# Kernel tuning notes

Hardware: AMD Instinct MI355X
Metric: run time of the kernel (lower is better)

Reference implementation:

```python
import jax, jax.numpy as jnp
import numpy as np

FEAT_DIM = 2048
H_DIM = 1024
N = 8192  # num_obj (tree nodes in pre-order traversal order)


def setup_inputs() -> dict:
    key = jax.random.key(0)
    ks = jax.random.split(key, 5)
    features = jax.random.normal(ks[0], (N, FEAT_DIM), dtype=jnp.float32)
    # block_orthogonal init approximated by scaled gaussian (same math at runtime)
    Wx = jax.random.normal(ks[1], (4 * H_DIM, FEAT_DIM), dtype=jnp.float32) / np.sqrt(FEAT_DIM)
    Wh = jax.random.normal(ks[2], (4 * H_DIM, H_DIM), dtype=jnp.float32) / np.sqrt(H_DIM)
    bx = jnp.zeros((4 * H_DIM,), dtype=jnp.float32)
    # iofuh bias: forget-gate block [2h:3h] filled with 1.0
    bh = jnp.zeros((4 * H_DIM,), dtype=jnp.float32).at[2 * H_DIM:3 * H_DIM].set(1.0)
    # binary tree in pre-order-compatible (topological) order: parent of t is (t-1)//2 < t; root = -1
    t = jnp.arange(N)
    parent_idx = jnp.where(t == 0, -1, (t - 1) // 2).astype(jnp.int32)
    root_c = jax.random.normal(ks[3], (1, H_DIM), dtype=jnp.float32)
    root_h = jax.random.normal(ks[4], (1, H_DIM), dtype=jnp.float32)
    return {"features": features, "Wx": Wx, "bx": bx, "Wh": Wh, "bh": bh,
            "parent_idx": parent_idx, "root_c": root_c, "root_h": root_h}


def reference(features, Wx, bx, Wh, bh, parent_idx, root_c, root_h):
    # Precompute the input projection for ALL nodes with one big GEMM
    # (the original does this per-node; math is identical).
    xproj = features @ Wx.T + (bx + bh)  # [N, 4H]
    WhT = Wh.T  # [H, 4H]
    # state buffers; slot 0 holds the root state, slot t+1 holds node t's state
    h_buf = jnp.concatenate([root_h, jnp.zeros((N, H_DIM), features.dtype)], axis=0)  # [N+1, H]
    c_buf = jnp.concatenate([root_c, jnp.zeros((N, H_DIM), features.dtype)], axis=0)

    def step(carry, inp):
        h_buf, c_buf = carry
        t, p, xp = inp
        hp = h_buf[p + 1]  # parent hidden [H]
        cp = c_buf[p + 1]  # parent cell   [H]
        iofu = xp + hp @ WhT  # [4H]
        i, o, f, u = jnp.split(iofu, 4)
        i = jax.nn.sigmoid(i)
        o = jax.nn.sigmoid(o)
        f = jax.nn.sigmoid(f)
        u = jnp.tanh(u)
        c = i * u + f * cp
        h = o * jnp.tanh(c)
        h_buf = h_buf.at[t + 1].set(h)
        c_buf = c_buf.at[t + 1].set(c)
        return (h_buf, c_buf), h

    ts = jnp.arange(N)
    (_, _), hidden = jax.lax.scan(step, (h_buf, c_buf), (ts, parent_idx, xproj))
    return hidden  # [N, H] == treelstm_io.hidden rows in traversal order
```

## Files before the change

kernel.cpp:

```cpp
#include <hip/hip_runtime.h>
#include <math.h>

#define FEAT 2048
#define HD 1024
#define FH 4096
#define NN 8192

using s16x8 = __attribute__((ext_vector_type(8))) short;
using f32x4 = __attribute__((ext_vector_type(4))) float;

#define GLOBAL_AS __attribute__((address_space(1)))
#define LDS_AS __attribute__((address_space(3)))

__device__ __forceinline__ void gload_lds16(const void* g, void* l) {
    __builtin_amdgcn_global_load_lds((const GLOBAL_AS unsigned int*)g,
                                     (LDS_AS unsigned int*)l, 16, 0, 0);
}

__device__ __forceinline__ unsigned short f2bf(float f) {
    union { float f; unsigned u; } v; v.f = f;
    unsigned r = v.u + 0x7FFFu + ((v.u >> 16) & 1u);
    return (unsigned short)(r >> 16);
}

__device__ __forceinline__ float fast_sig(float x) { return 1.0f / (1.0f + __expf(-x)); }
__device__ __forceinline__ float fast_tanh(float x) {
    float ax = fabsf(x);
    float e = __expf(2.0f * ax);
    float r = 1.0f - 2.0f / (e + 1.0f);
    return copysignf(r, x);
}

__global__ __launch_bounds__(256) void convert_all_kernel(
    const float* __restrict__ feat, const float* __restrict__ Wx,
    const float* __restrict__ Wh, unsigned short* __restrict__ feat_b,
    unsigned short* __restrict__ Wx_b, unsigned short* __restrict__ Wh_b)
{
    const size_t n1 = (size_t)NN * FEAT;
    const size_t n2 = n1 + (size_t)FH * FEAT;
    size_t i = ((size_t)blockIdx.x * 256 + threadIdx.x) * 8;
    const float* s; unsigned short* d;
    if (i < n1)      { s = feat + i;        d = feat_b + i; }
    else if (i < n2) { s = Wx + (i - n1);   d = Wx_b + (i - n1); }
    else             { s = Wh + (i - n2);   d = Wh_b + (i - n2); }
    float4 a = *(const float4*)s;
    float4 b = *(const float4*)(s + 4);
    unsigned short r[8] = {f2bf(a.x), f2bf(a.y), f2bf(a.z), f2bf(a.w),
                           f2bf(b.x), f2bf(b.y), f2bf(b.z), f2bf(b.w)};
    *(s16x8*)d = *(const s16x8*)r;
}

__global__ __launch_bounds__(256) void init_kernel(
    const float* __restrict__ root_h, const float* __restrict__ root_c,
    unsigned short* __restrict__ h_buf, float* __restrict__ c_buf)
{
    const int i = blockIdx.x * 256 + threadIdx.x;
    if (i < HD) { h_buf[i] = f2bf(root_h[i]); c_buf[i] = root_c[i]; }
}

__global__ __launch_bounds__(256) void xproj_mfma(
    const unsigned short* __restrict__ Ab,
    const unsigned short* __restrict__ Bb,
    const float* __restrict__ bx, const float* __restrict__ bh,
    float* __restrict__ xproj)
{
    __shared__ unsigned short As[128 * 32];
    __shared__ unsigned short Bs[128 * 32];
    const int tid = threadIdx.x;
    const int wid = tid >> 6;
    const int lane = tid & 63;
    const int bm = blockIdx.x * 128;
    const int bn = blockIdx.y * 128;
    const int wm = (wid & 1) * 64;
    const int wn = (wid >> 1) * 64;

    const int srow = wid * 16 + (lane >> 2);
    const int sk = (lane & 3) * 8;
    const unsigned short* gA0 = Ab + (size_t)(bm + srow) * FEAT + sk;
    const unsigned short* gA1 = Ab + (size_t)(bm + 64 + srow) * FEAT + sk;
    const unsigned short* gB0 = Bb + (size_t)(bn + srow) * FEAT + sk;
    const unsigned short* gB1 = Bb + (size_t)(bn + 64 + srow) * FEAT + sk;
    unsigned short* lA0 = As + wid * 512;
    unsigned short* lA1 = As + 2048 + wid * 512;
    unsigned short* lB0 = Bs + wid * 512;
    unsigned short* lB1 = Bs + 2048 + wid * 512;

    f32x4 acc[4][4];
    #pragma unroll
    for (int i = 0; i < 4; ++i)
        #pragma unroll
        for (int j = 0; j < 4; ++j) { f32x4 z = {0.f, 0.f, 0.f, 0.f}; acc[i][j] = z; }

    const int fr = lane & 15;
    const int fk = (lane >> 4) * 8;

    for (int k0 = 0; k0 < FEAT; k0 += 32) {
        gload_lds16(gA0 + k0, lA0);
        gload_lds16(gA1 + k0, lA1);
        gload_lds16(gB0 + k0, lB0);
        gload_lds16(gB1 + k0, lB1);
        __syncthreads();

        s16x8 aF[4], bF[4];
        #pragma unroll
        for (int i = 0; i < 4; ++i)
            aF[i] = *(const s16x8*)&As[(wm + i * 16 + fr) * 32 + fk];
        #pragma unroll
        for (int j = 0; j < 4; ++j)
            bF[j] = *(const s16x8*)&Bs[(wn + j * 16 + fr) * 32 + fk];
        #pragma unroll
        for (int i = 0; i < 4; ++i)
            #pragma unroll
            for (int j = 0; j < 4; ++j)
                acc[i][j] = __builtin_amdgcn_mfma_f32_16x16x32_bf16(aF[i], bF[j], acc[i][j], 0, 0, 0);
        __syncthreads();
    }

    const int fq = lane >> 4;
    #pragma unroll
    for (int j = 0; j < 4; ++j) {
        const int col = bn + wn + j * 16 + fr;
        const float bias = bx[col] + bh[col];
        #pragma unroll
        for (int i = 0; i < 4; ++i) {
            const int rowb = bm + wm + i * 16 + fq * 4;
            #pragma unroll
            for (int reg = 0; reg < 4; ++reg)
                xproj[(size_t)(rowb + reg) * FH + col] = acc[i][j][reg] + bias;
        }
    }
}

__device__ __forceinline__ void level_epilogue(
    f32x4 (&acc)[4][4], const float* __restrict__ xproj,
    const int* __restrict__ parent, unsigned short* __restrict__ h_buf,
    float* __restrict__ c_buf, float* __restrict__ out,
    int t0, int lim, int wm, int col, int fq)
{
    #pragma unroll
    for (int i = 0; i < 4; ++i) {
        #pragma unroll
        for (int reg = 0; reg < 4; ++reg) {
            const int t = t0 + wm + i * 16 + fq * 4 + reg;
            if (t < lim) {
                const int p = parent[t];
                const size_t xb = (size_t)t * FH + col;
                const float gi = acc[i][0][reg] + xproj[xb];
                const float go = acc[i][1][reg] + xproj[xb + HD];
                const float gf = acc[i][2][reg] + xproj[xb + 2 * HD];
                const float gu = acc[i][3][reg] + xproj[xb + 3 * HD];
                const float cp = c_buf[(size_t)(p + 1) * HD + col];
                const float c = fast_sig(gi) * fast_tanh(gu) + fast_sig(gf) * cp;
                const float h = fast_sig(go) * fast_tanh(c);
                c_buf[(size_t)(t + 1) * HD + col] = c;
                h_buf[(size_t)(t + 1) * HD + col] = f2bf(h);
                out[(size_t)t * HD + col] = h;
            }
        }
    }
}

__device__ __forceinline__ void bk128_issue(
    const unsigned short* const (&gA)[8], const unsigned short* const (&gB)[8],
    int k0, unsigned short* As, unsigned short* Bs, int wbase)
{
    #pragma unroll
    for (int q = 0; q < 8; ++q) {
        gload_lds16(gA[q] + k0, (char*)As + q * 4096 + wbase);
        gload_lds16(gB[q] + k0, (char*)Bs + q * 4096 + wbase);
    }
}

__device__ __forceinline__ void bk128_compute(
    const unsigned short* As, const unsigned short* Bs,
    f32x4 (&acc)[4][4], int wm, int wn16, int fr, int fkb)
{
    #pragma unroll
    for (int kk = 0; kk < 4; ++kk) {
        s16x8 aF[4], bF[4];
        #pragma unroll
        for (int i = 0; i < 4; ++i) {
            const int r = wm + i * 16 + fr;
            const int byteIn = (kk * 64 + fkb) ^ ((r & 7) << 4);
            aF[i] = *(const s16x8*)((const char*)As + r * 256 + byteIn);
        }
        #pragma unroll
        for (int g = 0; g < 4; ++g) {
            const int r = g * 32 + wn16 + fr;
            const int byteIn = (kk * 64 + fkb) ^ ((r & 7) << 4);
            bF[g] = *(const s16x8*)((const char*)Bs + r * 256 + byteIn);
        }
        #pragma unroll
        for (int i = 0; i < 4; ++i)
            #pragma unroll
            for (int g = 0; g < 4; ++g)
                acc[i][g] = __builtin_amdgcn_mfma_f32_16x16x32_bf16(aF[i], bF[g], acc[i][g], 0, 0, 0);
    }
}

__global__ __launch_bounds__(256) void level_bk128_dbuf(
    const float* __restrict__ xproj, const unsigned short* __restrict__ Whb,
    const int* __restrict__ parent, unsigned short* __restrict__ h_buf,
    float* __restrict__ c_buf, float* __restrict__ out,
    int start, int count)
{
    __shared__ unsigned short As0[128 * 128];
    __shared__ unsigned short Bs0[128 * 128];
    __shared__ unsigned short As1[128 * 128];
    __shared__ unsigned short Bs1[128 * 128];
    const int tid = threadIdx.x;
    const int wid = tid >> 6;
    const int lane = tid & 63;
    const int t0 = start + blockIdx.x * 128;
    const int jg0 = blockIdx.y * 32;
    const int lim = start + count;
    const int wm = (wid & 1) * 64;
    const int wn16 = (wid >> 1) * 16;
    const int wbase = wid * 1024;
    const int srow_b = tid >> 4;
    const int rowbyte = (tid & 15) * 16;

    const unsigned short* gA[8];
    const unsigned short* gB[8];
    #pragma unroll
    for (int q = 0; q < 8; ++q) {
        const int r = q * 16 + srow_b;
        const int sk = (rowbyte ^ ((r & 7) << 4)) >> 1;
        const int tA = min(t0 + r, lim - 1);
        gA[q] = h_buf + (size_t)(parent[tA] + 1) * HD + sk;
        const int whrow = ((r >> 5) << 10) + jg0 + (r & 31);
        gB[q] = Whb + (size_t)whrow * HD + sk;
    }

    f32x4 acc[4][4];
    #pragma unroll
    for (int i = 0; i < 4; ++i)
        #pragma unroll
        for (int g = 0; g < 4; ++g) { f32x4 z = {0.f, 0.f, 0.f, 0.f}; acc[i][g] = z; }

    const int fr = lane & 15;
    const int fkb = (lane >> 4) * 16;

    bk128_issue(gA, gB, 0, As0, Bs0, wbase);
    #pragma unroll
    for (int t = 0; t < 8; ++t) {
        unsigned short* curA = (t & 1) ? As1 : As0;
        unsigned short* curB = (t & 1) ? Bs1 : Bs0;
        unsigned short* nxtA = (t & 1) ? As0 : As1;
        unsigned short* nxtB = (t & 1) ? Bs0 : Bs1;
        if (t < 7) {
            bk128_issue(gA, gB, (t + 1) * 128, nxtA, nxtB, wbase);
            asm volatile("s_waitcnt vmcnt(16)" ::: "memory");
        } else {
            asm volatile("s_waitcnt vmcnt(0)" ::: "memory");
        }
        __builtin_amdgcn_s_barrier();
        __builtin_amdgcn_sched_barrier(0);
        bk128_compute(curA, curB, acc, wm, wn16, fr, fkb);
        __builtin_amdgcn_sched_barrier(0);
        __builtin_amdgcn_s_barrier();
    }

    level_epilogue(acc, xproj, parent, h_buf, c_buf, out,
                   t0, lim, wm, jg0 + wn16 + fr, lane >> 4);
}

__global__ __launch_bounds__(256) void level_mfma(
    const float* __restrict__ xproj, const unsigned short* __restrict__ Whb,
    const int* __restrict__ parent, unsigned short* __restrict__ h_buf,
    float* __restrict__ c_buf, float* __restrict__ out,
    int start, int count)
{
    __shared__ unsigned short As[128 * 32];
    __shared__ unsigned short Bs[128 * 32];
    const int tid = threadIdx.x;
    const int wid = tid >> 6;
    const int lane = tid & 63;
    const int t0 = start + blockIdx.x * 128;
    const int jg0 = blockIdx.y * 32;
    const int lim = start + count;
    const int wm = (wid & 1) * 64;
    const int wn16 = (wid >> 1) * 16;

    const int srow = wid * 16 + (lane >> 2);
    const int sk = (lane & 3) * 8;
    const int tA0 = min(t0 + srow, lim - 1);
    const int tA1 = min(t0 + 64 + srow, lim - 1);
    const unsigned short* gA0 = h_buf + (size_t)(parent[tA0] + 1) * HD + sk;
    const unsigned short* gA1 = h_buf + (size_t)(parent[tA1] + 1) * HD + sk;
    const int r0 = srow, r1 = 64 + srow;
    const unsigned short* gB0 = Whb + (size_t)((r0 >> 5) * HD + jg0 + (r0 & 31)) * HD + sk;
    const unsigned short* gB1 = Whb + (size_t)((r1 >> 5) * HD + jg0 + (r1 & 31)) * HD + sk;
    unsigned short* lA0 = As + wid * 512;
    unsigned short* lA1 = As + 2048 + wid * 512;
    unsigned short* lB0 = Bs + wid * 512;
    unsigned short* lB1 = Bs + 2048 + wid * 512;

    f32x4 acc[4][4];
    #pragma unroll
    for (int i = 0; i < 4; ++i)
        #pragma unroll
        for (int g = 0; g < 4; ++g) { f32x4 z = {0.f, 0.f, 0.f, 0.f}; acc[i][g] = z; }

    const int fr = lane & 15;
    const int fk = (lane >> 4) * 8;

    for (int k0 = 0; k0 < HD; k0 += 32) {
        gload_lds16(gA0 + k0, lA0);
        gload_lds16(gA1 + k0, lA1);
        gload_lds16(gB0 + k0, lB0);
        gload_lds16(gB1 + k0, lB1);
        __syncthreads();

        s16x8 aF[4], bF[4];
        #pragma unroll
        for (int i = 0; i < 4; ++i)
            aF[i] = *(const s16x8*)&As[(wm + i * 16 + fr) * 32 + fk];
        #pragma unroll
        for (int g = 0; g < 4; ++g)
            bF[g] = *(const s16x8*)&Bs[(g * 32 + wn16 + fr) * 32 + fk];
        #pragma unroll
        for (int i = 0; i < 4; ++i)
            #pragma unroll
            for (int g = 0; g < 4; ++g)
                acc[i][g] = __builtin_amdgcn_mfma_f32_16x16x32_bf16(aF[i], bF[g], acc[i][g], 0, 0, 0);
        __syncthreads();
    }

    level_epilogue(acc, xproj, parent, h_buf, c_buf, out,
                   t0, lim, wm, jg0 + wn16 + fr, lane >> 4);
}

extern "C" void kernel_launch(void* const* d_in, const int* in_sizes, int n_in,
                              void* d_out, int out_size, void* d_ws, size_t ws_size,
                              hipStream_t stream) {
    const float* feat   = (const float*)d_in[0];
    const float* Wx     = (const float*)d_in[1];
    const float* bx     = (const float*)d_in[2];
    const float* Wh     = (const float*)d_in[3];
    const float* bh     = (const float*)d_in[4];
    const int*   parent = (const int*)d_in[5];
    const float* root_c = (const float*)d_in[6];
    const float* root_h = (const float*)d_in[7];
    float* out = (float*)d_out;

    char* ws = (char*)d_ws;
    float* xproj = (float*)ws;                          ws += (size_t)NN * FH * 4;
    float* c_buf = (float*)ws;                          ws += (size_t)(NN + 1) * HD * 4;
    unsigned short* feat_b = (unsigned short*)ws;       ws += (size_t)NN * FEAT * 2;
    unsigned short* Wx_b = (unsigned short*)ws;         ws += (size_t)FH * FEAT * 2;
    unsigned short* Wh_b = (unsigned short*)ws;         ws += (size_t)FH * HD * 2;
    unsigned short* h_buf = (unsigned short*)ws;        ws += (size_t)(NN + 1) * HD * 2;

    const size_t ntot = (size_t)NN * FEAT + (size_t)FH * FEAT + (size_t)FH * HD;
    convert_all_kernel<<<(unsigned)(ntot / 8 / 256), 256, 0, stream>>>(
        feat, Wx, Wh, feat_b, Wx_b, Wh_b);
    init_kernel<<<4, 256, 0, stream>>>(root_h, root_c, h_buf, c_buf);

    dim3 g1(NN / 128, FH / 128);
    xproj_mfma<<<g1, 256, 0, stream>>>(feat_b, Wx_b, bx, bh, xproj);

    for (int start = 0, sz = 1; start < NN; start += sz, sz *= 2) {
        const int count = (sz < NN - start) ? sz : (NN - start);
        dim3 g2((count + 127) / 128, HD / 32);
        if (count >= 1024)
            level_mfma<<<g2, 256, 0, stream>>>(xproj, Wh_b, parent, h_buf, c_buf,
                                               out, start, count);
        else
            level_bk128_dbuf<<<g2, 256, 0, stream>>>(xproj, Wh_b, parent, h_buf,
                                                     c_buf, out, start, count);
    }
}
```

Before: 531.2 us.

## Rewrite input-projection GEMM with 256x256 tiles, double-buffered swizzled LDS pipeline

Replaces the 128x128 single-buffered xproj GEMM with a 512-thread, 256x256-tile kernel that uses 128KB of LDS split into two buffers. The next K-slab is prefetched into the other buffer while MFMAs run across four phases, with XOR-swizzled LDS addressing and raised wave priority around the MFMA sections. The aims are to hide global-load latency, cut LDS bank conflicts and improve data reuse per tile. The cost is more registers and LDS per block, which means fewer resident blocks and fewer blocks overall (32x16).

```diff
diff --git a/kernel.cpp b/kernel.cpp
--- a/kernel.cpp
+++ b/kernel.cpp
@@ -58,72 +58,111 @@
     if (i < HD) { h_buf[i] = f2bf(root_h[i]); c_buf[i] = root_c[i]; }
 }
 
-__global__ __launch_bounds__(256) void xproj_mfma(
+__global__ __launch_bounds__(512, 2) void xproj_8ph(
     const unsigned short* __restrict__ Ab,
     const unsigned short* __restrict__ Bb,
     const float* __restrict__ bx, const float* __restrict__ bh,
     float* __restrict__ xproj)
 {
-    __shared__ unsigned short As[128 * 32];
-    __shared__ unsigned short Bs[128 * 32];
+    __shared__ char lds[131072];
     const int tid = threadIdx.x;
     const int wid = tid >> 6;
     const int lane = tid & 63;
-    const int bm = blockIdx.x * 128;
-    const int bn = blockIdx.y * 128;
-    const int wm = (wid & 1) * 64;
-    const int wn = (wid >> 1) * 64;
-
-    const int srow = wid * 16 + (lane >> 2);
-    const int sk = (lane & 3) * 8;
-    const unsigned short* gA0 = Ab + (size_t)(bm + srow) * FEAT + sk;
-    const unsigned short* gA1 = Ab + (size_t)(bm + 64 + srow) * FEAT + sk;
-    const unsigned short* gB0 = Bb + (size_t)(bn + srow) * FEAT + sk;
-    const unsigned short* gB1 = Bb + (size_t)(bn + 64 + srow) * FEAT + sk;
-    unsigned short* lA0 = As + wid * 512;
-    unsigned short* lA1 = As + 2048 + wid * 512;
-    unsigned short* lB0 = Bs + wid * 512;
-    unsigned short* lB1 = Bs + 2048 + wid * 512;
-
-    f32x4 acc[4][4];
-    #pragma unroll
-    for (int i = 0; i < 4; ++i)
+    const int wr = wid >> 2;
+    const int wc = wid & 3;
+    const int bm = blockIdx.x * 256;
+    const int bn = blockIdx.y * 256;
+    const int fr = lane & 15;
+    const int fq = lane >> 4;
+
+    const int srow = tid >> 3;
+    const int sslot = (tid & 7) ^ (srow & 7);
+    const unsigned short* gA[4];
+    const unsigned short* gB[4];
+    #pragma unroll
+    for (int q = 0; q < 4; ++q) {
+        gA[q] = Ab + (size_t)(bm + q * 64 + srow) * FEAT + sslot * 8;
+        gB[q] = Bb + (size_t)(bn + q * 64 + srow) * FEAT + sslot * 8;
+    }
+    const int ldsoff = tid * 16;
+
+    f32x4 acc[8][4];
+    #pragma unroll
+    for (int i = 0; i < 8; ++i)
         #pragma unroll
         for (int j = 0; j < 4; ++j) { f32x4 z = {0.f, 0.f, 0.f, 0.f}; acc[i][j] = z; }
 
-    const int fr = lane & 15;
-    const int fk = (lane >> 4) * 8;
-
-    for (int k0 = 0; k0 < FEAT; k0 += 32) {
-        gload_lds16(gA0 + k0, lA0);
-        gload_lds16(gA1 + k0, lA1);
-        gload_lds16(gB0 + k0, lB0);
-        gload_lds16(gB1 + k0, lB1);
-        __syncthreads();
-
-        s16x8 aF[4], bF[4];
-        #pragma unroll
-        for (int i = 0; i < 4; ++i)
-            aF[i] = *(const s16x8*)&As[(wm + i * 16 + fr) * 32 + fk];
-        #pragma unroll
-        for (int j = 0; j < 4; ++j)
-            bF[j] = *(const s16x8*)&Bs[(wn + j * 16 + fr) * 32 + fk];
-        #pragma unroll
-        for (int i = 0; i < 4; ++i)
-            #pragma unroll
-            for (int j = 0; j < 4; ++j)
-                acc[i][j] = __builtin_amdgcn_mfma_f32_16x16x32_bf16(aF[i], bF[j], acc[i][j], 0, 0, 0);
-        __syncthreads();
-    }
-
-    const int fq = lane >> 4;
+    #pragma unroll
+    for (int q = 0; q < 4; ++q) {
+        gload_lds16(gA[q], lds + q * 8192 + ldsoff);
+        gload_lds16(gB[q], lds + 32768 + q * 8192 + ldsoff);
+    }
+    asm volatile("s_waitcnt vmcnt(0)" ::: "memory");
+    __builtin_amdgcn_s_barrier();
+
+    for (int t = 0; t < 32; ++t) {
+        const int d = t & 1;
+        const char* LA = lds + d * 65536;
+        const char* LB = LA + 32768;
+        char* SA = lds + (d ^ 1) * 65536;
+        char* SB = SA + 32768;
+        const int knext = (t + 1) * 64;
+
+        #pragma unroll
+        for (int p = 0; p < 4; ++p) {
+            const int mh = p >> 1, nh = p & 1;
+            s16x8 aF[4][2], bF[2][2];
+            #pragma unroll
+            for (int i = 0; i < 4; ++i) {
+                const int row = wr * 128 + (mh * 4 + i) * 16 + fr;
+                #pragma unroll
+                for (int kk = 0; kk < 2; ++kk) {
+                    const int kbyte = kk * 64 + fq * 16;
+                    aF[i][kk] = *(const s16x8*)(LA + row * 128 + (kbyte ^ ((row & 7) << 4)));
+                }
+            }
+            #pragma unroll
+            for (int j = 0; j < 2; ++j) {
+                const int row = wc * 64 + (nh * 2 + j) * 16 + fr;
+                #pragma unroll
+                for (int kk = 0; kk < 2; ++kk) {
+                    const int kbyte = kk * 64 + fq * 16;
+                    bF[j][kk] = *(const s16x8*)(LB + row * 128 + (kbyte ^ ((row & 7) << 4)));
+                }
+            }
+            if (t < 31 && p < 2) {
+                gload_lds16(gA[2 * p] + knext,     SA + (2 * p) * 8192 + ldsoff);
+                gload_lds16(gB[2 * p] + knext,     SB + (2 * p) * 8192 + ldsoff);
+                gload_lds16(gA[2 * p + 1] + knext, SA + (2 * p + 1) * 8192 + ldsoff);
+                gload_lds16(gB[2 * p + 1] + knext, SB + (2 * p + 1) * 8192 + ldsoff);
+            }
+            __builtin_amdgcn_s_barrier();
+            __builtin_amdgcn_s_setprio(1);
+            #pragma unroll
+            for (int i = 0; i < 4; ++i)
+                #pragma unroll
+                for (int j = 0; j < 2; ++j)
+                    #pragma unroll
+                    for (int kk = 0; kk < 2; ++kk)
+                        acc[mh * 4 + i][nh * 2 + j] = __builtin_amdgcn_mfma_f32_16x16x32_bf16(
+                            aF[i][kk], bF[j][kk], acc[mh * 4 + i][nh * 2 + j], 0, 0, 0);
+            __builtin_amdgcn_s_setprio(0);
+            if (p < 3) {
+                __builtin_amdgcn_s_barrier();
+            } else {
+                asm volatile("s_waitcnt vmcnt(0)" ::: "memory");
+                __builtin_amdgcn_s_barrier();
+            }
+        }
+    }
+
     #pragma unroll
     for (int j = 0; j < 4; ++j) {
-        const int col = bn + wn + j * 16 + fr;
+        const int col = bn + wc * 64 + j * 16 + fr;
         const float bias = bx[col] + bh[col];
         #pragma unroll
-        for (int i = 0; i < 4; ++i) {
-            const int rowb = bm + wm + i * 16 + fq * 4;
+        for (int i = 0; i < 8; ++i) {
+            const int rowb = bm + wr * 128 + i * 16 + fq * 4;
             #pragma unroll
             for (int reg = 0; reg < 4; ++reg)
                 xproj[(size_t)(rowb + reg) * FH + col] = acc[i][j][reg] + bias;
@@ -357,8 +396,8 @@
         feat, Wx, Wh, feat_b, Wx_b, Wh_b);
     init_kernel<<<4, 256, 0, stream>>>(root_h, root_c, h_buf, c_buf);
 
-    dim3 g1(NN / 128, FH / 128);
-    xproj_mfma<<<g1, 256, 0, stream>>>(feat_b, Wx_b, bx, bh, xproj);
+    dim3 g1(NN / 256, FH / 256);
+    xproj_8ph<<<g1, 512, 0, stream>>>(feat_b, Wx_b, bx, bh, xproj);
 
     for (int start = 0, sz = 1; start < NN; start += sz, sz *= 2) {
         const int count = (sz < NN - start) ? sz : (NN - start);
```

Measured after the change: 511.3 us. -3.7%, faster.
